# Optimization experiments

Hardware: AMD Instinct MI355X
Metric: run time of the kernel (lower is better)

The kernel has to match this reference:

```python
import jax, jax.numpy as jnp
import numpy as np

WINDOW_SIZE = 64
SHIFT_SIZE = WINDOW_SIZE // 2  # shift_windows=True
HEAD_DIM = 64
SCALE = HEAD_DIM ** (-0.5)


def _shift_mask(W):
    # static shift-window mask, computed with numpy (all shapes static)
    img_mask = np.zeros((W,), dtype=np.float32)
    cnt = 0
    for s in (slice(0, -WINDOW_SIZE), slice(-WINDOW_SIZE, -SHIFT_SIZE), slice(-SHIFT_SIZE, None)):
        img_mask[s] = cnt
        cnt += 1
    mw = img_mask.reshape(W // WINDOW_SIZE, WINDOW_SIZE)  # (num_win, ws)
    mask = mw[:, None, :] - mw[:, :, None]                # (num_win, ws, ws)
    mask = np.where(mask != 0.0, -100.0, 0.0).astype(np.float32)
    return jnp.asarray(mask)


def setup_inputs() -> dict:
    key = jax.random.key(0)
    k1, k2, k3, k4 = jax.random.split(key, 4)
    B, W, C = 32, 8192, HEAD_DIM
    return {
        "q": jax.random.normal(k1, (B, W, C), dtype=jnp.float32),
        "k": jax.random.normal(k2, (B, W, C), dtype=jnp.float32),
        "v": jax.random.normal(k3, (B, W, C), dtype=jnp.float32),
        "rel_pos_table": jax.random.normal(k4, (2 * WINDOW_SIZE - 1, 1), dtype=jnp.float32) * 0.02,
    }


def reference(q, k, v, rel_pos_table):
    B, W, C = q.shape
    ws = WINDOW_SIZE
    # relative position bias gather: (1, ws, ws)
    coords = jnp.arange(ws)
    rel_idx = coords[None, :] * 0 + (coords[:, None] - coords[None, :]) + (ws - 1)  # (ws, ws)
    bias = rel_pos_table[rel_idx.reshape(-1)].reshape(ws, ws, -1)
    bias = jnp.transpose(bias, (2, 0, 1))  # (1, ws, ws)

    mask = _shift_mask(W)  # (num_win, ws, ws)

    # cyclic shift
    q = jnp.roll(q, shift=-SHIFT_SIZE, axis=1)
    k = jnp.roll(k, shift=-SHIFT_SIZE, axis=1)
    v = jnp.roll(v, shift=-SHIFT_SIZE, axis=1)

    # window partition -> (B * num_win, ws, C)
    num_win = W // ws
    qw = q.reshape(B * num_win, ws, C)
    kw = k.reshape(B * num_win, ws, C)
    vw = v.reshape(B * num_win, ws, C)

    attn = jnp.einsum('bnc,bmc->bnm', qw, kw) * SCALE + bias  # (B*nw, ws, ws)
    attn = attn.reshape(B, num_win, ws, ws) + mask[None]
    attn = attn.reshape(-1, ws, ws)
    attn = jax.nn.softmax(attn, axis=-1)

    xw = jnp.einsum('bnm,bmc->bnc', attn, vw)  # (B*nw, ws, C)
    x = xw.reshape(B, W, C)
    x = jnp.roll(x, shift=SHIFT_SIZE, axis=1)
    return (x, attn)
```

## Files before the change

### kernel.cpp

```cpp
#include <hip/hip_runtime.h>
#include <cstdint>
#include <cstddef>

#define WS 64
#define SHIFT 32
#define WTOT 8192
#define NWIN 128
#define SCALE_F 0.125f

typedef __bf16 bf16x8 __attribute__((ext_vector_type(8)));
typedef unsigned short u16x8 __attribute__((ext_vector_type(8)));
typedef unsigned short u16x4 __attribute__((ext_vector_type(4)));
typedef float f32x4 __attribute__((ext_vector_type(4)));

__device__ __forceinline__ unsigned short f2bf(float f) {
  unsigned int u = __builtin_bit_cast(unsigned int, f);
  u += 0x7FFFu + ((u >> 16) & 1u);
  return (unsigned short)(u >> 16);
}
__device__ __forceinline__ float bf2f(unsigned short h) {
  unsigned int u = ((unsigned int)h) << 16;
  return __builtin_bit_cast(float, u);
}

__device__ __forceinline__ int swz(int row, int col) {
  return (row * WS + col) ^ (((row >> 1) & 7) << 3);
}

__global__ __launch_bounds__(256, 5) void win_attn(
    const float* __restrict__ q, const float* __restrict__ k,
    const float* __restrict__ v, const float* __restrict__ table,
    float* __restrict__ xout, float* __restrict__ attn_out) {
  __shared__ __align__(16) unsigned short s_khi[WS * WS];
  __shared__ __align__(16) unsigned short s_klo[WS * WS];
  __shared__ __align__(16) unsigned short s_vthi[WS * WS];
  __shared__ __align__(16) unsigned short s_vtlo[WS * WS];

  const int t = threadIdx.x;
  const int b = blockIdx.x;
  const int batch = b >> 7;
  const int win = b & (NWIN - 1);
  const int lane = t & 63;
  const int wave = t >> 6;
  const int lrow = lane & 15;
  const int quad = lane >> 4;

  {
    const int lr = t >> 2;
    const int lc = (t & 3) << 4;
    const int grow = (win * WS + lr + SHIFT) & (WTOT - 1);
    const float* kp = k + ((size_t)batch * WTOT + grow) * WS + lc;
#pragma unroll
    for (int s = 0; s < 2; ++s) {
      const float4 x0 = *(const float4*)(kp + 8 * s);
      const float4 x1 = *(const float4*)(kp + 8 * s + 4);
      const float a[8] = {x0.x, x0.y, x0.z, x0.w, x1.x, x1.y, x1.z, x1.w};
      u16x8 hi, lo;
#pragma unroll
      for (int e = 0; e < 8; ++e) {
        const unsigned short h = f2bf(a[e]);
        hi[e] = h;
        lo[e] = f2bf(a[e] - bf2f(h));
      }
      const int idx = swz(lr, lc + 8 * s);
      *(u16x8*)(s_khi + idx) = hi;
      *(u16x8*)(s_klo + idx) = lo;
    }
  }

  {
    const int m0 = (t >> 4) << 2;
    const int c0 = (t & 15) << 2;
    float4 vr[4];
#pragma unroll
    for (int j = 0; j < 4; ++j) {
      const int grow = (win * WS + m0 + j + SHIFT) & (WTOT - 1);
      vr[j] = *(const float4*)(v + ((size_t)batch * WTOT + grow) * WS + c0);
    }
    const float vb[4][4] = {{vr[0].x, vr[0].y, vr[0].z, vr[0].w},
                            {vr[1].x, vr[1].y, vr[1].z, vr[1].w},
                            {vr[2].x, vr[2].y, vr[2].z, vr[2].w},
                            {vr[3].x, vr[3].y, vr[3].z, vr[3].w}};
#pragma unroll
    for (int e = 0; e < 4; ++e) {
      u16x4 hi, lo;
#pragma unroll
      for (int j = 0; j < 4; ++j) {
        const unsigned short h = f2bf(vb[j][e]);
        hi[j] = h;
        lo[j] = f2bf(vb[j][e] - bf2f(h));
      }
      const int idx = swz(c0 + e, m0);
      *(u16x4*)(s_vthi + idx) = hi;
      *(u16x4*)(s_vtlo + idx) = lo;
    }
  }

  bf16x8 qfhi[2], qflo[2];
  {
    const int grow = (win * WS + wave * 16 + lrow + SHIFT) & (WTOT - 1);
    const float* qp = q + ((size_t)batch * WTOT + grow) * WS + quad * 8;
#pragma unroll
    for (int kh = 0; kh < 2; ++kh) {
      const float4 x0 = *(const float4*)(qp + kh * 32);
      const float4 x1 = *(const float4*)(qp + kh * 32 + 4);
      const float a[8] = {x0.x, x0.y, x0.z, x0.w, x1.x, x1.y, x1.z, x1.w};
      u16x8 hi, lo;
#pragma unroll
      for (int e = 0; e < 8; ++e) {
        const unsigned short h = f2bf(a[e]);
        hi[e] = h;
        lo[e] = f2bf(a[e] - bf2f(h));
      }
      qfhi[kh] = __builtin_bit_cast(bf16x8, hi);
      qflo[kh] = __builtin_bit_cast(bf16x8, lo);
    }
  }

  float biasr[4][4];
  {
    const bool masked = (win == NWIN - 1);
    const float* tb = table + (WS - 1);
#pragma unroll
    for (int reg = 0; reg < 4; ++reg) {
      const int r = wave * 16 + quad * 4 + reg;
#pragma unroll
      for (int j = 0; j < 4; ++j) {
        const int m = j * 16 + lrow;
        float bv = __ldg(tb + (r - m));
        if (masked && (((r ^ m) & 32) != 0)) bv -= 100.0f;
        biasr[reg][j] = bv;
      }
    }
  }
  __syncthreads();

  const f32x4 z4 = {0.f, 0.f, 0.f, 0.f};
  f32x4 acc[4] = {z4, z4, z4, z4};
#pragma unroll
  for (int kh = 0; kh < 2; ++kh) {
    const int k0 = kh * 32 + quad * 8;
    const bf16x8 ahi = qfhi[kh];
    const bf16x8 alo = qflo[kh];
#pragma unroll
    for (int j = 0; j < 4; ++j) {
      const int idx = swz(j * 16 + lrow, k0);
      const bf16x8 bhi = *(const bf16x8*)(s_khi + idx);
      const bf16x8 blo = *(const bf16x8*)(s_klo + idx);
      acc[j] = __builtin_amdgcn_mfma_f32_16x16x32_bf16(ahi, bhi, acc[j], 0, 0, 0);
      acc[j] = __builtin_amdgcn_mfma_f32_16x16x32_bf16(alo, bhi, acc[j], 0, 0, 0);
      acc[j] = __builtin_amdgcn_mfma_f32_16x16x32_bf16(ahi, blo, acc[j], 0, 0, 0);
    }
  }

  float p[4][4];
#pragma unroll
  for (int reg = 0; reg < 4; ++reg) {
    float val[4];
    float vmax = -1e30f;
#pragma unroll
    for (int j = 0; j < 4; ++j) {
      const float s = acc[j][reg] * SCALE_F + biasr[reg][j];
      val[j] = s;
      vmax = fmaxf(vmax, s);
    }
#pragma unroll
    for (int off = 1; off < 16; off <<= 1)
      vmax = fmaxf(vmax, __shfl_xor(vmax, off, 64));
    float sum = 0.f;
#pragma unroll
    for (int j = 0; j < 4; ++j) {
      val[j] = __expf(val[j] - vmax);
      sum += val[j];
    }
#pragma unroll
    for (int off = 1; off < 16; off <<= 1)
      sum += __shfl_xor(sum, off, 64);
    const float inv = 1.0f / sum;
#pragma unroll
    for (int j = 0; j < 4; ++j) p[reg][j] = val[j] * inv;
  }

  __syncthreads();

  {
    float* arow = attn_out + (size_t)b * (WS * WS);
#pragma unroll
    for (int reg = 0; reg < 4; ++reg) {
      const int r = wave * 16 + quad * 4 + reg;
#pragma unroll
      for (int j = 0; j < 4; ++j) {
        const int m = j * 16 + lrow;
        const float pv = p[reg][j];
        arow[r * WS + m] = pv;
        const unsigned short h = f2bf(pv);
        const int idx = swz(r, m);
        s_khi[idx] = h;
        s_klo[idx] = f2bf(pv - bf2f(h));
      }
    }
  }
  __syncthreads();

  f32x4 xacc[4] = {z4, z4, z4, z4};
#pragma unroll
  for (int kh = 0; kh < 2; ++kh) {
    const int k0 = kh * 32 + quad * 8;
    const int aidx = swz(wave * 16 + lrow, k0);
    const bf16x8 phi = *(const bf16x8*)(s_khi + aidx);
    const bf16x8 plo = *(const bf16x8*)(s_klo + aidx);
#pragma unroll
    for (int j = 0; j < 4; ++j) {
      const int idx = swz(j * 16 + lrow, k0);
      const bf16x8 vhi = *(const bf16x8*)(s_vthi + idx);
      const bf16x8 vlo = *(const bf16x8*)(s_vtlo + idx);
      xacc[j] = __builtin_amdgcn_mfma_f32_16x16x32_bf16(phi, vhi, xacc[j], 0, 0, 0);
      xacc[j] = __builtin_amdgcn_mfma_f32_16x16x32_bf16(plo, vhi, xacc[j], 0, 0, 0);
      xacc[j] = __builtin_amdgcn_mfma_f32_16x16x32_bf16(phi, vlo, xacc[j], 0, 0, 0);
    }
  }

#pragma unroll
  for (int reg = 0; reg < 4; ++reg) {
    const int r = wave * 16 + quad * 4 + reg;
    const int gr = (win * WS + r + SHIFT) & (WTOT - 1);
    float* xrow = xout + ((size_t)batch * WTOT + gr) * WS;
#pragma unroll
    for (int j = 0; j < 4; ++j) {
      xrow[j * 16 + lrow] = xacc[j][reg];
    }
  }
}

extern "C" void kernel_launch(void* const* d_in, const int* in_sizes, int n_in,
                              void* d_out, int out_size, void* d_ws, size_t ws_size,
                              hipStream_t stream) {
  (void)in_sizes; (void)n_in; (void)out_size; (void)d_ws; (void)ws_size;
  const float* q = (const float*)d_in[0];
  const float* k = (const float*)d_in[1];
  const float* v = (const float*)d_in[2];
  const float* table = (const float*)d_in[3];
  float* xout = (float*)d_out;
  float* attn = (float*)d_out + (size_t)32 * WTOT * WS;
  win_attn<<<dim3(4096), dim3(256), 0, stream>>>(q, k, v, table, xout, attn);
}
```

Baseline: 280.4 us.

## Stage attn probs and output through LDS for vectorized float4 global stores

The softmax probabilities are written as fp32 into a swizzled LDS tile that aliases the K buffers. They are read back row-wise for float4 global stores of attn, and re-read per wave to build the bf16 hi/lo A fragments for the PV MFMA. The output x is staged the same way, replacing scattered scalar stores with coalesced float4 stores. One __syncthreads is dropped because each wave only touches its own 16 rows. Manual bf16 rounding is also swapped for native __bf16 conversions, which may compile to hardware convert instructions.

```diff
diff --git a/kernel.cpp b/kernel.cpp
--- a/kernel.cpp
+++ b/kernel.cpp
@@ -9,32 +9,28 @@
 #define SCALE_F 0.125f
 
 typedef __bf16 bf16x8 __attribute__((ext_vector_type(8)));
-typedef unsigned short u16x8 __attribute__((ext_vector_type(8)));
-typedef unsigned short u16x4 __attribute__((ext_vector_type(4)));
+typedef __bf16 bf16x4 __attribute__((ext_vector_type(4)));
 typedef float f32x4 __attribute__((ext_vector_type(4)));
 
-__device__ __forceinline__ unsigned short f2bf(float f) {
-  unsigned int u = __builtin_bit_cast(unsigned int, f);
-  u += 0x7FFFu + ((u >> 16) & 1u);
-  return (unsigned short)(u >> 16);
-}
-__device__ __forceinline__ float bf2f(unsigned short h) {
-  unsigned int u = ((unsigned int)h) << 16;
-  return __builtin_bit_cast(float, u);
-}
-
-__device__ __forceinline__ int swz(int row, int col) {
+__device__ __forceinline__ int swz16(int row, int col) {
   return (row * WS + col) ^ (((row >> 1) & 7) << 3);
+}
+
+__device__ __forceinline__ int swz32(int row, int col) {
+  const int q2 = (row >> 2) & 3;
+  return row * WS + (col ^ (((q2 & 1) << 4) | ((q2 >> 1) << 2)));
 }
 
 __global__ __launch_bounds__(256, 5) void win_attn(
     const float* __restrict__ q, const float* __restrict__ k,
     const float* __restrict__ v, const float* __restrict__ table,
     float* __restrict__ xout, float* __restrict__ attn_out) {
-  __shared__ __align__(16) unsigned short s_khi[WS * WS];
-  __shared__ __align__(16) unsigned short s_klo[WS * WS];
-  __shared__ __align__(16) unsigned short s_vthi[WS * WS];
-  __shared__ __align__(16) unsigned short s_vtlo[WS * WS];
+  __shared__ __align__(16) unsigned short s_mem[4 * WS * WS];
+  unsigned short* const s_khi  = s_mem;
+  unsigned short* const s_klo  = s_mem + WS * WS;
+  unsigned short* const s_vthi = s_mem + 2 * WS * WS;
+  unsigned short* const s_vtlo = s_mem + 3 * WS * WS;
+  float* const s_p = (float*)s_mem;
 
   const int t = threadIdx.x;
   const int b = blockIdx.x;
@@ -55,16 +51,16 @@
       const float4 x0 = *(const float4*)(kp + 8 * s);
       const float4 x1 = *(const float4*)(kp + 8 * s + 4);
       const float a[8] = {x0.x, x0.y, x0.z, x0.w, x1.x, x1.y, x1.z, x1.w};
-      u16x8 hi, lo;
+      bf16x8 hv, lv;
 #pragma unroll
       for (int e = 0; e < 8; ++e) {
-        const unsigned short h = f2bf(a[e]);
-        hi[e] = h;
-        lo[e] = f2bf(a[e] - bf2f(h));
-      }
-      const int idx = swz(lr, lc + 8 * s);
-      *(u16x8*)(s_khi + idx) = hi;
-      *(u16x8*)(s_klo + idx) = lo;
+        const __bf16 h = (__bf16)a[e];
+        hv[e] = h;
+        lv[e] = (__bf16)(a[e] - (float)h);
+      }
+      const int idx = swz16(lr, lc + 8 * s);
+      *(bf16x8*)(s_khi + idx) = hv;
+      *(bf16x8*)(s_klo + idx) = lv;
     }
   }
 
@@ -83,16 +79,17 @@
                             {vr[3].x, vr[3].y, vr[3].z, vr[3].w}};
 #pragma unroll
     for (int e = 0; e < 4; ++e) {
-      u16x4 hi, lo;
+      bf16x4 hv, lv;
 #pragma unroll
       for (int j = 0; j < 4; ++j) {
-        const unsigned short h = f2bf(vb[j][e]);
-        hi[j] = h;
-        lo[j] = f2bf(vb[j][e] - bf2f(h));
-      }
-      const int idx = swz(c0 + e, m0);
-      *(u16x4*)(s_vthi + idx) = hi;
-      *(u16x4*)(s_vtlo + idx) = lo;
+        const float x = vb[j][e];
+        const __bf16 h = (__bf16)x;
+        hv[j] = h;
+        lv[j] = (__bf16)(x - (float)h);
+      }
+      const int idx = swz16(c0 + e, m0);
+      *(bf16x4*)(s_vthi + idx) = hv;
+      *(bf16x4*)(s_vtlo + idx) = lv;
     }
   }
 
@@ -105,15 +102,15 @@
       const float4 x0 = *(const float4*)(qp + kh * 32);
       const float4 x1 = *(const float4*)(qp + kh * 32 + 4);
       const float a[8] = {x0.x, x0.y, x0.z, x0.w, x1.x, x1.y, x1.z, x1.w};
-      u16x8 hi, lo;
+      bf16x8 hv, lv;
 #pragma unroll
       for (int e = 0; e < 8; ++e) {
-        const unsigned short h = f2bf(a[e]);
-        hi[e] = h;
-        lo[e] = f2bf(a[e] - bf2f(h));
-      }
-      qfhi[kh] = __builtin_bit_cast(bf16x8, hi);
-      qflo[kh] = __builtin_bit_cast(bf16x8, lo);
+        const __bf16 h = (__bf16)a[e];
+        hv[e] = h;
+        lv[e] = (__bf16)(a[e] - (float)h);
+      }
+      qfhi[kh] = hv;
+      qflo[kh] = lv;
     }
   }
 
@@ -144,7 +141,7 @@
     const bf16x8 alo = qflo[kh];
 #pragma unroll
     for (int j = 0; j < 4; ++j) {
-      const int idx = swz(j * 16 + lrow, k0);
+      const int idx = swz16(j * 16 + lrow, k0);
       const bf16x8 bhi = *(const bf16x8*)(s_khi + idx);
       const bf16x8 blo = *(const bf16x8*)(s_klo + idx);
       acc[j] = __builtin_amdgcn_mfma_f32_16x16x32_bf16(ahi, bhi, acc[j], 0, 0, 0);
@@ -183,35 +180,43 @@
 
   __syncthreads();
 
-  {
-    float* arow = attn_out + (size_t)b * (WS * WS);
-#pragma unroll
-    for (int reg = 0; reg < 4; ++reg) {
-      const int r = wave * 16 + quad * 4 + reg;
-#pragma unroll
-      for (int j = 0; j < 4; ++j) {
-        const int m = j * 16 + lrow;
-        const float pv = p[reg][j];
-        arow[r * WS + m] = pv;
-        const unsigned short h = f2bf(pv);
-        const int idx = swz(r, m);
-        s_khi[idx] = h;
-        s_klo[idx] = f2bf(pv - bf2f(h));
-      }
-    }
-  }
-  __syncthreads();
+#pragma unroll
+  for (int reg = 0; reg < 4; ++reg) {
+    const int r = wave * 16 + quad * 4 + reg;
+#pragma unroll
+    for (int j = 0; j < 4; ++j) {
+      s_p[swz32(r, j * 16 + lrow)] = p[reg][j];
+    }
+  }
+
+  {
+    const int r = wave * 16 + lrow;
+    float* arow = attn_out + (size_t)b * (WS * WS) + (size_t)r * WS;
+#pragma unroll
+    for (int i = 0; i < 4; ++i) {
+      const int c = i * 16 + quad * 4;
+      *(float4*)(arow + c) = *(const float4*)(s_p + swz32(r, c));
+    }
+  }
 
   f32x4 xacc[4] = {z4, z4, z4, z4};
 #pragma unroll
   for (int kh = 0; kh < 2; ++kh) {
-    const int k0 = kh * 32 + quad * 8;
-    const int aidx = swz(wave * 16 + lrow, k0);
-    const bf16x8 phi = *(const bf16x8*)(s_khi + aidx);
-    const bf16x8 plo = *(const bf16x8*)(s_klo + aidx);
-#pragma unroll
-    for (int j = 0; j < 4; ++j) {
-      const int idx = swz(j * 16 + lrow, k0);
+    const int c0 = kh * 32 + quad * 8;
+    const int r = wave * 16 + lrow;
+    const float4 a0 = *(const float4*)(s_p + swz32(r, c0));
+    const float4 a1 = *(const float4*)(s_p + swz32(r, c0 + 4));
+    const float pa[8] = {a0.x, a0.y, a0.z, a0.w, a1.x, a1.y, a1.z, a1.w};
+    bf16x8 phi, plo;
+#pragma unroll
+    for (int e = 0; e < 8; ++e) {
+      const __bf16 h = (__bf16)pa[e];
+      phi[e] = h;
+      plo[e] = (__bf16)(pa[e] - (float)h);
+    }
+#pragma unroll
+    for (int j = 0; j < 4; ++j) {
+      const int idx = swz16(j * 16 + lrow, c0);
       const bf16x8 vhi = *(const bf16x8*)(s_vthi + idx);
       const bf16x8 vlo = *(const bf16x8*)(s_vtlo + idx);
       xacc[j] = __builtin_amdgcn_mfma_f32_16x16x32_bf16(phi, vhi, xacc[j], 0, 0, 0);
@@ -223,11 +228,19 @@
 #pragma unroll
   for (int reg = 0; reg < 4; ++reg) {
     const int r = wave * 16 + quad * 4 + reg;
+#pragma unroll
+    for (int j = 0; j < 4; ++j) {
+      s_p[swz32(r, j * 16 + lrow)] = xacc[j][reg];
+    }
+  }
+  {
+    const int r = wave * 16 + lrow;
     const int gr = (win * WS + r + SHIFT) & (WTOT - 1);
     float* xrow = xout + ((size_t)batch * WTOT + gr) * WS;
 #pragma unroll
-    for (int j = 0; j < 4; ++j) {
-      xrow[j * 16 + lrow] = xacc[j][reg];
+    for (int i = 0; i < 4; ++i) {
+      const int c = i * 16 + quad * 4;
+      *(float4*)(xrow + c) = *(const float4*)(s_p + swz32(r, c));
     }
   }
 }
```

Result: no change. 280.7 us (+0.1%).

## Process eight windows per block with register-prefetched loads and double-buffered LDS

Applied to the files above, without the earlier changes.

Each block of the now-persistent-style grid loops over eight windows instead of one. It prefetches the next window's q/k/v into registers while computing the current one and ping-pongs between two LDS buffers. The bias table load is hoisted out of the loop, and bf16 conversion uses native casts instead of manual bit tricks. The goal is to hide global-load latency and amortize setup. In exchange, occupancy drops to 2 blocks/CU with a smaller grid of 512 blocks, which may leave CUs underused on a 256-CU device.

```diff
diff --git a/kernel.cpp b/kernel.cpp
--- a/kernel.cpp
+++ b/kernel.cpp
@@ -6,230 +6,258 @@
 #define SHIFT 32
 #define WTOT 8192
 #define NWIN 128
+#define NWPB 8
+#define NBLK 512
 #define SCALE_F 0.125f
 
 typedef __bf16 bf16x8 __attribute__((ext_vector_type(8)));
-typedef unsigned short u16x8 __attribute__((ext_vector_type(8)));
-typedef unsigned short u16x4 __attribute__((ext_vector_type(4)));
+typedef __bf16 bf16x4 __attribute__((ext_vector_type(4)));
 typedef float f32x4 __attribute__((ext_vector_type(4)));
 
-__device__ __forceinline__ unsigned short f2bf(float f) {
-  unsigned int u = __builtin_bit_cast(unsigned int, f);
-  u += 0x7FFFu + ((u >> 16) & 1u);
-  return (unsigned short)(u >> 16);
-}
-__device__ __forceinline__ float bf2f(unsigned short h) {
-  unsigned int u = ((unsigned int)h) << 16;
-  return __builtin_bit_cast(float, u);
-}
-
-__device__ __forceinline__ int swz(int row, int col) {
+__device__ __forceinline__ int swz16(int row, int col) {
   return (row * WS + col) ^ (((row >> 1) & 7) << 3);
 }
 
-__global__ __launch_bounds__(256, 5) void win_attn(
+__global__ __launch_bounds__(256, 2) void win_attn(
     const float* __restrict__ q, const float* __restrict__ k,
     const float* __restrict__ v, const float* __restrict__ table,
     float* __restrict__ xout, float* __restrict__ attn_out) {
-  __shared__ __align__(16) unsigned short s_khi[WS * WS];
-  __shared__ __align__(16) unsigned short s_klo[WS * WS];
-  __shared__ __align__(16) unsigned short s_vthi[WS * WS];
-  __shared__ __align__(16) unsigned short s_vtlo[WS * WS];
+  __shared__ __align__(16) unsigned short s_mem[2][4 * WS * WS];
 
   const int t = threadIdx.x;
-  const int b = blockIdx.x;
-  const int batch = b >> 7;
-  const int win = b & (NWIN - 1);
+  const int bid = blockIdx.x;
   const int lane = t & 63;
   const int wave = t >> 6;
   const int lrow = lane & 15;
   const int quad = lane >> 4;
 
-  {
-    const int lr = t >> 2;
-    const int lc = (t & 3) << 4;
-    const int grow = (win * WS + lr + SHIFT) & (WTOT - 1);
-    const float* kp = k + ((size_t)batch * WTOT + grow) * WS + lc;
-#pragma unroll
-    for (int s = 0; s < 2; ++s) {
-      const float4 x0 = *(const float4*)(kp + 8 * s);
-      const float4 x1 = *(const float4*)(kp + 8 * s + 4);
-      const float a[8] = {x0.x, x0.y, x0.z, x0.w, x1.x, x1.y, x1.z, x1.w};
-      u16x8 hi, lo;
-#pragma unroll
-      for (int e = 0; e < 8; ++e) {
-        const unsigned short h = f2bf(a[e]);
-        hi[e] = h;
-        lo[e] = f2bf(a[e] - bf2f(h));
-      }
-      const int idx = swz(lr, lc + 8 * s);
-      *(u16x8*)(s_khi + idx) = hi;
-      *(u16x8*)(s_klo + idx) = lo;
-    }
-  }
-
-  {
-    const int m0 = (t >> 4) << 2;
-    const int c0 = (t & 15) << 2;
-    float4 vr[4];
-#pragma unroll
-    for (int j = 0; j < 4; ++j) {
-      const int grow = (win * WS + m0 + j + SHIFT) & (WTOT - 1);
-      vr[j] = *(const float4*)(v + ((size_t)batch * WTOT + grow) * WS + c0);
-    }
-    const float vb[4][4] = {{vr[0].x, vr[0].y, vr[0].z, vr[0].w},
-                            {vr[1].x, vr[1].y, vr[1].z, vr[1].w},
-                            {vr[2].x, vr[2].y, vr[2].z, vr[2].w},
-                            {vr[3].x, vr[3].y, vr[3].z, vr[3].w}};
-#pragma unroll
-    for (int e = 0; e < 4; ++e) {
-      u16x4 hi, lo;
-#pragma unroll
-      for (int j = 0; j < 4; ++j) {
-        const unsigned short h = f2bf(vb[j][e]);
-        hi[j] = h;
-        lo[j] = f2bf(vb[j][e] - bf2f(h));
-      }
-      const int idx = swz(c0 + e, m0);
-      *(u16x4*)(s_vthi + idx) = hi;
-      *(u16x4*)(s_vtlo + idx) = lo;
-    }
-  }
-
-  bf16x8 qfhi[2], qflo[2];
-  {
-    const int grow = (win * WS + wave * 16 + lrow + SHIFT) & (WTOT - 1);
-    const float* qp = q + ((size_t)batch * WTOT + grow) * WS + quad * 8;
-#pragma unroll
-    for (int kh = 0; kh < 2; ++kh) {
-      const float4 x0 = *(const float4*)(qp + kh * 32);
-      const float4 x1 = *(const float4*)(qp + kh * 32 + 4);
-      const float a[8] = {x0.x, x0.y, x0.z, x0.w, x1.x, x1.y, x1.z, x1.w};
-      u16x8 hi, lo;
-#pragma unroll
-      for (int e = 0; e < 8; ++e) {
-        const unsigned short h = f2bf(a[e]);
-        hi[e] = h;
-        lo[e] = f2bf(a[e] - bf2f(h));
-      }
-      qfhi[kh] = __builtin_bit_cast(bf16x8, hi);
-      qflo[kh] = __builtin_bit_cast(bf16x8, lo);
-    }
-  }
+  const int klr = t >> 2;
+  const int klc = (t & 3) << 4;
+  const int vm0 = (t >> 4) << 2;
+  const int vc0 = (t & 15) << 2;
 
   float biasr[4][4];
   {
-    const bool masked = (win == NWIN - 1);
     const float* tb = table + (WS - 1);
 #pragma unroll
     for (int reg = 0; reg < 4; ++reg) {
       const int r = wave * 16 + quad * 4 + reg;
 #pragma unroll
       for (int j = 0; j < 4; ++j) {
-        const int m = j * 16 + lrow;
-        float bv = __ldg(tb + (r - m));
-        if (masked && (((r ^ m) & 32) != 0)) bv -= 100.0f;
-        biasr[reg][j] = bv;
+        biasr[reg][j] = __ldg(tb + (r - (j * 16 + lrow)));
       }
     }
   }
-  __syncthreads();
-
-  const f32x4 z4 = {0.f, 0.f, 0.f, 0.f};
-  f32x4 acc[4] = {z4, z4, z4, z4};
-#pragma unroll
-  for (int kh = 0; kh < 2; ++kh) {
-    const int k0 = kh * 32 + quad * 8;
-    const bf16x8 ahi = qfhi[kh];
-    const bf16x8 alo = qflo[kh];
-#pragma unroll
-    for (int j = 0; j < 4; ++j) {
-      const int idx = swz(j * 16 + lrow, k0);
-      const bf16x8 bhi = *(const bf16x8*)(s_khi + idx);
-      const bf16x8 blo = *(const bf16x8*)(s_klo + idx);
-      acc[j] = __builtin_amdgcn_mfma_f32_16x16x32_bf16(ahi, bhi, acc[j], 0, 0, 0);
-      acc[j] = __builtin_amdgcn_mfma_f32_16x16x32_bf16(alo, bhi, acc[j], 0, 0, 0);
-      acc[j] = __builtin_amdgcn_mfma_f32_16x16x32_bf16(ahi, blo, acc[j], 0, 0, 0);
-    }
+
+  float4 L[2][12];
+
+#define ISSUE(W)                                                          \
+  {                                                                       \
+    const int wid_ = bid * NWPB + (W);                                    \
+    const int ba_ = wid_ >> 7;                                            \
+    const int wi_ = wid_ & (NWIN - 1);                                    \
+    const size_t base_ = (size_t)ba_ * WTOT;                              \
+    const int qr_ = (wi_ * WS + wave * 16 + lrow + SHIFT) & (WTOT - 1);   \
+    const float* qp_ = q + (base_ + qr_) * WS + quad * 8;                 \
+    L[(W) & 1][0] = *(const float4*)(qp_);                                \
+    L[(W) & 1][1] = *(const float4*)(qp_ + 4);                            \
+    L[(W) & 1][2] = *(const float4*)(qp_ + 32);                           \
+    L[(W) & 1][3] = *(const float4*)(qp_ + 36);                           \
+    const int kr_ = (wi_ * WS + klr + SHIFT) & (WTOT - 1);                \
+    const float* kp_ = k + (base_ + kr_) * WS + klc;                      \
+    L[(W) & 1][4] = *(const float4*)(kp_);                                \
+    L[(W) & 1][5] = *(const float4*)(kp_ + 4);                            \
+    L[(W) & 1][6] = *(const float4*)(kp_ + 8);                            \
+    L[(W) & 1][7] = *(const float4*)(kp_ + 12);                           \
+    const int vr0_ = (wi_ * WS + vm0 + 0 + SHIFT) & (WTOT - 1);           \
+    const int vr1_ = (wi_ * WS + vm0 + 1 + SHIFT) & (WTOT - 1);           \
+    const int vr2_ = (wi_ * WS + vm0 + 2 + SHIFT) & (WTOT - 1);           \
+    const int vr3_ = (wi_ * WS + vm0 + 3 + SHIFT) & (WTOT - 1);           \
+    L[(W) & 1][8]  = *(const float4*)(v + (base_ + vr0_) * WS + vc0);     \
+    L[(W) & 1][9]  = *(const float4*)(v + (base_ + vr1_) * WS + vc0);     \
+    L[(W) & 1][10] = *(const float4*)(v + (base_ + vr2_) * WS + vc0);     \
+    L[(W) & 1][11] = *(const float4*)(v + (base_ + vr3_) * WS + vc0);     \
   }
 
-  float p[4][4];
-#pragma unroll
-  for (int reg = 0; reg < 4; ++reg) {
-    float val[4];
-    float vmax = -1e30f;
-#pragma unroll
-    for (int j = 0; j < 4; ++j) {
-      const float s = acc[j][reg] * SCALE_F + biasr[reg][j];
-      val[j] = s;
-      vmax = fmaxf(vmax, s);
-    }
-#pragma unroll
-    for (int off = 1; off < 16; off <<= 1)
-      vmax = fmaxf(vmax, __shfl_xor(vmax, off, 64));
-    float sum = 0.f;
-#pragma unroll
-    for (int j = 0; j < 4; ++j) {
-      val[j] = __expf(val[j] - vmax);
-      sum += val[j];
-    }
-#pragma unroll
-    for (int off = 1; off < 16; off <<= 1)
-      sum += __shfl_xor(sum, off, 64);
-    const float inv = 1.0f / sum;
-#pragma unroll
-    for (int j = 0; j < 4; ++j) p[reg][j] = val[j] * inv;
-  }
-
-  __syncthreads();
-
-  {
-    float* arow = attn_out + (size_t)b * (WS * WS);
+  ISSUE(0);
+
+#pragma unroll
+  for (int w = 0; w < NWPB; ++w) {
+    const int s = w & 1;
+    unsigned short* const s_khi  = s_mem[s];
+    unsigned short* const s_klo  = s_mem[s] + WS * WS;
+    unsigned short* const s_vthi = s_mem[s] + 2 * WS * WS;
+    unsigned short* const s_vtlo = s_mem[s] + 3 * WS * WS;
+
+    const int wid = bid * NWPB + w;
+    const int batch = wid >> 7;
+    const int win = wid & (NWIN - 1);
+    const bool masked = (win == NWIN - 1);
+    const size_t base = (size_t)batch * WTOT;
+
+    if (w + 1 < NWPB) ISSUE(w + 1);
+
+    {
+      const float a[16] = {L[s][4].x, L[s][4].y, L[s][4].z, L[s][4].w,
+                           L[s][5].x, L[s][5].y, L[s][5].z, L[s][5].w,
+                           L[s][6].x, L[s][6].y, L[s][6].z, L[s][6].w,
+                           L[s][7].x, L[s][7].y, L[s][7].z, L[s][7].w};
+#pragma unroll
+      for (int h = 0; h < 2; ++h) {
+        bf16x8 hv, lv;
+#pragma unroll
+        for (int e = 0; e < 8; ++e) {
+          const float x = a[8 * h + e];
+          const __bf16 hh = (__bf16)x;
+          hv[e] = hh;
+          lv[e] = (__bf16)(x - (float)hh);
+        }
+        const int idx = swz16(klr, klc + 8 * h);
+        *(bf16x8*)(s_khi + idx) = hv;
+        *(bf16x8*)(s_klo + idx) = lv;
+      }
+    }
+    {
+      const float vb[4][4] = {
+          {L[s][8].x,  L[s][8].y,  L[s][8].z,  L[s][8].w},
+          {L[s][9].x,  L[s][9].y,  L[s][9].z,  L[s][9].w},
+          {L[s][10].x, L[s][10].y, L[s][10].z, L[s][10].w},
+          {L[s][11].x, L[s][11].y, L[s][11].z, L[s][11].w}};
+#pragma unroll
+      for (int e = 0; e < 4; ++e) {
+        bf16x4 hv, lv;
+#pragma unroll
+        for (int j = 0; j < 4; ++j) {
+          const float x = vb[j][e];
+          const __bf16 hh = (__bf16)x;
+          hv[j] = hh;
+          lv[j] = (__bf16)(x - (float)hh);
+        }
+        const int idx = swz16(vc0 + e, vm0);
+        *(bf16x4*)(s_vthi + idx) = hv;
+        *(bf16x4*)(s_vtlo + idx) = lv;
+      }
+    }
+    bf16x8 qfhi[2], qflo[2];
+#pragma unroll
+    for (int kh = 0; kh < 2; ++kh) {
+      const float a[8] = {L[s][2 * kh].x,     L[s][2 * kh].y,
+                          L[s][2 * kh].z,     L[s][2 * kh].w,
+                          L[s][2 * kh + 1].x, L[s][2 * kh + 1].y,
+                          L[s][2 * kh + 1].z, L[s][2 * kh + 1].w};
+      bf16x8 hv, lv;
+#pragma unroll
+      for (int e = 0; e < 8; ++e) {
+        const __bf16 hh = (__bf16)a[e];
+        hv[e] = hh;
+        lv[e] = (__bf16)(a[e] - (float)hh);
+      }
+      qfhi[kh] = hv;
+      qflo[kh] = lv;
+    }
+
+    __syncthreads();
+
+    const f32x4 z4 = {0.f, 0.f, 0.f, 0.f};
+    f32x4 acc[4] = {z4, z4, z4, z4};
+#pragma unroll
+    for (int kh = 0; kh < 2; ++kh) {
+      const int k0 = kh * 32 + quad * 8;
+      const bf16x8 ahi = qfhi[kh];
+      const bf16x8 alo = qflo[kh];
+#pragma unroll
+      for (int j = 0; j < 4; ++j) {
+        const int idx = swz16(j * 16 + lrow, k0);
+        const bf16x8 bhi = *(const bf16x8*)(s_khi + idx);
+        const bf16x8 blo = *(const bf16x8*)(s_klo + idx);
+        acc[j] = __builtin_amdgcn_mfma_f32_16x16x32_bf16(ahi, bhi, acc[j], 0, 0, 0);
+        acc[j] = __builtin_amdgcn_mfma_f32_16x16x32_bf16(alo, bhi, acc[j], 0, 0, 0);
+        acc[j] = __builtin_amdgcn_mfma_f32_16x16x32_bf16(ahi, blo, acc[j], 0, 0, 0);
+      }
+    }
+
+    float p[4][4];
 #pragma unroll
     for (int reg = 0; reg < 4; ++reg) {
       const int r = wave * 16 + quad * 4 + reg;
+      float val[4];
+      float vmax = -1e30f;
 #pragma unroll
       for (int j = 0; j < 4; ++j) {
         const int m = j * 16 + lrow;
-        const float pv = p[reg][j];
-        arow[r * WS + m] = pv;
-        const unsigned short h = f2bf(pv);
-        const int idx = swz(r, m);
-        s_khi[idx] = h;
-        s_klo[idx] = f2bf(pv - bf2f(h));
+        float sv = acc[j][reg] * SCALE_F + biasr[reg][j];
+        if (masked && (((r ^ m) & 32) != 0)) sv -= 100.0f;
+        val[j] = sv;
+        vmax = fmaxf(vmax, sv);
+      }
+#pragma unroll
+      for (int off = 1; off < 16; off <<= 1)
+        vmax = fmaxf(vmax, __shfl_xor(vmax, off, 64));
+      float sum = 0.f;
+#pragma unroll
+      for (int j = 0; j < 4; ++j) {
+        val[j] = __expf(val[j] - vmax);
+        sum += val[j];
+      }
+#pragma unroll
+      for (int off = 1; off < 16; off <<= 1)
+        sum += __shfl_xor(sum, off, 64);
+      const float inv = 1.0f / sum;
+#pragma unroll
+      for (int j = 0; j < 4; ++j) p[reg][j] = val[j] * inv;
+    }
+
+    __syncthreads();
+
+    {
+      float* arow = attn_out + (size_t)wid * (WS * WS);
+#pragma unroll
+      for (int reg = 0; reg < 4; ++reg) {
+        const int r = wave * 16 + quad * 4 + reg;
+#pragma unroll
+        for (int j = 0; j < 4; ++j) {
+          const int m = j * 16 + lrow;
+          const float pv = p[reg][j];
+          arow[r * WS + m] = pv;
+          const __bf16 hh = (__bf16)pv;
+          const int idx = swz16(r, m);
+          *(__bf16*)(s_khi + idx) = hh;
+          *(__bf16*)(s_klo + idx) = (__bf16)(pv - (float)hh);
+        }
+      }
+    }
+    __syncthreads();
+
+    f32x4 xacc[4] = {z4, z4, z4, z4};
+#pragma unroll
+    for (int kh = 0; kh < 2; ++kh) {
+      const int k0 = kh * 32 + quad * 8;
+      const int aidx = swz16(wave * 16 + lrow, k0);
+      const bf16x8 phi = *(const bf16x8*)(s_khi + aidx);
+      const bf16x8 plo = *(const bf16x8*)(s_klo + aidx);
+#pragma unroll
+      for (int j = 0; j < 4; ++j) {
+        const int idx = swz16(j * 16 + lrow, k0);
+        const bf16x8 vhi = *(const bf16x8*)(s_vthi + idx);
+        const bf16x8 vlo = *(const bf16x8*)(s_vtlo + idx);
+        xacc[j] = __builtin_amdgcn_mfma_f32_16x16x32_bf16(phi, vhi, xacc[j], 0, 0, 0);
+        xacc[j] = __builtin_amdgcn_mfma_f32_16x16x32_bf16(plo, vhi, xacc[j], 0, 0, 0);
+        xacc[j] = __builtin_amdgcn_mfma_f32_16x16x32_bf16(phi, vlo, xacc[j], 0, 0, 0);
+      }
+    }
+
+#pragma unroll
+    for (int reg = 0; reg < 4; ++reg) {
+      const int r = wave * 16 + quad * 4 + reg;
+      const int gr = (win * WS + r + SHIFT) & (WTOT - 1);
+      float* xrow = xout + (base + gr) * WS;
+#pragma unroll
+      for (int j = 0; j < 4; ++j) {
+        xrow[j * 16 + lrow] = xacc[j][reg];
       }
     }
   }
-  __syncthreads();
-
-  f32x4 xacc[4] = {z4, z4, z4, z4};
-#pragma unroll
-  for (int kh = 0; kh < 2; ++kh) {
-    const int k0 = kh * 32 + quad * 8;
-    const int aidx = swz(wave * 16 + lrow, k0);
-    const bf16x8 phi = *(const bf16x8*)(s_khi + aidx);
-    const bf16x8 plo = *(const bf16x8*)(s_klo + aidx);
-#pragma unroll
-    for (int j = 0; j < 4; ++j) {
-      const int idx = swz(j * 16 + lrow, k0);
-      const bf16x8 vhi = *(const bf16x8*)(s_vthi + idx);
-      const bf16x8 vlo = *(const bf16x8*)(s_vtlo + idx);
-      xacc[j] = __builtin_amdgcn_mfma_f32_16x16x32_bf16(phi, vhi, xacc[j], 0, 0, 0);
-      xacc[j] = __builtin_amdgcn_mfma_f32_16x16x32_bf16(plo, vhi, xacc[j], 0, 0, 0);
-      xacc[j] = __builtin_amdgcn_mfma_f32_16x16x32_bf16(phi, vlo, xacc[j], 0, 0, 0);
-    }
-  }
-
-#pragma unroll
-  for (int reg = 0; reg < 4; ++reg) {
-    const int r = wave * 16 + quad * 4 + reg;
-    const int gr = (win * WS + r + SHIFT) & (WTOT - 1);
-    float* xrow = xout + ((size_t)batch * WTOT + gr) * WS;
-#pragma unroll
-    for (int j = 0; j < 4; ++j) {
-      xrow[j * 16 + lrow] = xacc[j][reg];
-    }
-  }
+#undef ISSUE
 }
 
 extern "C" void kernel_launch(void* const* d_in, const int* in_sizes, int n_in,
@@ -242,5 +270,5 @@
   const float* table = (const float*)d_in[3];
   float* xout = (float*)d_out;
   float* attn = (float*)d_out + (size_t)32 * WTOT * WS;
-  win_attn<<<dim3(4096), dim3(256), 0, stream>>>(q, k, v, table, xout, attn);
+  win_attn<<<dim3(NBLK), dim3(256), 0, stream>>>(q, k, v, table, xout, attn);
 }
```

Measured after the change: 290.9 us. +3.7%, slower.
